# Kernel tuning notes

Hardware: AMD Instinct MI355X
Metric: run time of the kernel (lower is better)

## Reference

```python
import jax, jax.numpy as jnp
import numpy as np

B, N, DIM_IN, DIM, DIM_C, RES, PAD, NBLK = 4, 32768, 3, 128, 128, 64, 0.1, 5
R2 = RES * RES
PLANES = ((0, 2), (0, 1), (1, 2))  # xz, xy, yz as in ConvONet


def setup_inputs() -> dict:
    key = jax.random.key(0)
    ks = jax.random.split(key, 8)
    x = jax.random.uniform(ks[0], (B, N, DIM_IN), minval=-0.55, maxval=0.55, dtype=jnp.float32)
    w = lambda k, sh: (jax.random.normal(k, sh, dtype=jnp.float32) * 0.02)
    return {
        "x": x,
        "stem_w": w(ks[1], (DIM_IN, 2 * DIM)), "stem_b": jnp.zeros((2 * DIM,), jnp.float32),
        "blk_fc0_w": w(ks[2], (NBLK, 2 * DIM, DIM)), "blk_fc0_b": jnp.zeros((NBLK, DIM), jnp.float32),
        "blk_fc1_w": w(ks[3], (NBLK, DIM, DIM)), "blk_fc1_b": jnp.zeros((NBLK, DIM), jnp.float32),
        "blk_sc_w": w(ks[4], (NBLK, 2 * DIM, DIM)), "blk_sc_b": jnp.zeros((NBLK, DIM), jnp.float32),
        "fc_c_w": w(ks[5], (DIM, DIM_C)), "fc_c_b": jnp.zeros((DIM_C,), jnp.float32),
    }


def _tri_indices(xyz):
    # per-plane flat grid index, ConvONet-style normalization with padding
    idxs = []
    for (a, b) in PLANES:
        p = xyz[..., (a, b)] / (1.0 + PAD + 1e-3) + 0.5
        p = jnp.clip(p, 0.0, 1.0 - 1e-6)
        ij = jnp.clip((p * RES).astype(jnp.int32), 0, RES - 1)
        idxs.append(ij[..., 0] + RES * ij[..., 1])  # (B, N)
    return idxs


def _scatter(c, idx, reduction):
    # c: (B, N, D), idx: (B, N) -> (B, R2, D)
    b, n, d = c.shape
    seg = (idx + jnp.arange(b, dtype=idx.dtype)[:, None] * R2).reshape(-1)
    flat = c.reshape(b * n, d)
    if reduction == "max":
        out = jax.ops.segment_max(flat, seg, num_segments=b * R2)
        out = jnp.where(jnp.isfinite(out), out, jnp.zeros((), c.dtype))  # empty cells -> 0
    else:  # mean
        s = jax.ops.segment_sum(flat, seg, num_segments=b * R2)
        cnt = jax.ops.segment_sum(jnp.ones((b * n, 1), c.dtype), seg, num_segments=b * R2)
        out = s / jnp.maximum(cnt, 1.0)
    return out.reshape(b, R2, d)


def _pool_local(h, idxs):
    # scatter-max into each triplane, gather back per-point, sum over the 3 planes
    out = jnp.zeros_like(h)
    for idx in idxs:
        grid = _scatter(h, idx, "max")                       # (B, R2, D)
        out = out + jnp.take_along_axis(grid, idx[..., None], axis=1)
    return out


def _block(h, w0, b0, w1, b1, ws, bs):
    # pre-activation residual MLP (ResnetBlockFC)
    net = jax.nn.relu(h) @ w0 + b0
    dx = jax.nn.relu(net) @ w1 + b1
    return h @ ws + bs + dx


def reference(x, stem_w, stem_b, blk_fc0_w, blk_fc0_b, blk_fc1_w, blk_fc1_b,
              blk_sc_w, blk_sc_b, fc_c_w, fc_c_b):
    xyz = x[..., :3]
    idxs = _tri_indices(xyz)
    h = x @ stem_w + stem_b                                  # (B, N, 2*DIM)
    h = _block(h, blk_fc0_w[0], blk_fc0_b[0], blk_fc1_w[0], blk_fc1_b[0], blk_sc_w[0], blk_sc_b[0])
    for i in range(1, NBLK):
        h = jnp.concatenate([h, _pool_local(h, idxs)], axis=-1)
        h = _block(h, blk_fc0_w[i], blk_fc0_b[i], blk_fc1_w[i], blk_fc1_b[i], blk_sc_w[i], blk_sc_b[i])
    c = h @ fc_c_w + fc_c_b                                  # (B, N, DIM_C)
    tri = jnp.stack([_scatter(c, idx, "mean") for idx in idxs])  # (3, B, R2, DIM_C)
    # flat index = i + RES*j -> reshape gives (j, i); move channels to front
    tri = tri.reshape(3, B, RES, RES, DIM_C).transpose(0, 1, 4, 2, 3)  # (3, B, DIM_C, RES, RES)
    return (xyz, c, tri)
```

## Files before the change

kernel.cpp:

```cpp
#include <hip/hip_runtime.h>
#include <hip/hip_bf16.h>

#define B_   4
#define NPTS 32768
#define BN   131072
#define RES  64
#define R2   4096
#define DIM  128
#define K2   256
#define NBLK 5
#define NSEG (3*B_*R2)

typedef __bf16 bf16x8 __attribute__((ext_vector_type(8)));
typedef float  f32x16 __attribute__((ext_vector_type(16)));
typedef unsigned int uintv4 __attribute__((ext_vector_type(4)));

#define MFMA(a,b,c) __builtin_amdgcn_mfma_f32_32x32x16_bf16((a),(b),(c),0,0,0)

#define O_IDX  0
#define O_CNT  (O_IDX + BN*16)
#define O_OFF  (O_CNT + NSEG*4)
#define O_WOFF (O_OFF + NSEG*4)
#define O_LIST (O_WOFF + NSEG*4)
#define O_H    (O_LIST + 3*BN*4)
#define O_GRID (O_H + BN*DIM*2)
#define O_W    (O_GRID + NSEG*DIM*2)
#define WBLK_ELEMS 81920

#define OUT_C_OFF   393216
#define OUT_TRI_OFF 17170432

__device__ __forceinline__ unsigned short f2bf(float f){
  unsigned int u = __float_as_uint(f);
  return (unsigned short)((u + 0x7fffu + ((u >> 16) & 1u)) >> 16);
}
__device__ __forceinline__ float bflo(unsigned int u){ return __uint_as_float(u << 16); }
__device__ __forceinline__ float bfhi(unsigned int u){ return __uint_as_float(u & 0xffff0000u); }
__device__ __forceinline__ int coord_bin(float u){
  float p = u / 1.101f + 0.5f;
  p = fminf(fmaxf(p, 0.0f), (float)(1.0 - 1e-6));
  int i = (int)(p * 64.0f);
  return i < 0 ? 0 : (i > 63 ? 63 : i);
}
__device__ __forceinline__ unsigned int pk_relu(unsigned int a){
  unsigned int r, z = 0;
  asm("v_pk_max_f16 %0, %1, %2" : "=v"(r) : "v"(a), "v"(z));
  return r;
}
__device__ __forceinline__ bf16x8 relu8(bf16x8 v){
  uintv4 u = __builtin_bit_cast(uintv4, v);
  u[0] = pk_relu(u[0]); u[1] = pk_relu(u[1]); u[2] = pk_relu(u[2]); u[3] = pk_relu(u[3]);
  return __builtin_bit_cast(bf16x8, u);
}

__global__ void k_prep(const float* __restrict__ x, float* __restrict__ out_xyz,
                       int* __restrict__ idx4, int* __restrict__ cnt){
  int p = blockIdx.x * 256 + threadIdx.x;
  if (p >= BN) return;
  float x0 = x[p*3+0], x1 = x[p*3+1], x2 = x[p*3+2];
  out_xyz[p*3+0] = x0; out_xyz[p*3+1] = x1; out_xyz[p*3+2] = x2;
  int b = p >> 15;
  int c0 = coord_bin(x0) + 64*coord_bin(x2);
  int c1 = coord_bin(x0) + 64*coord_bin(x1);
  int c2 = coord_bin(x1) + 64*coord_bin(x2);
  int4 c4; c4.x = c0; c4.y = c1; c4.z = c2; c4.w = 0;
  *(int4*)(idx4 + p*4) = c4;
  atomicAdd(&cnt[(0*B_+b)*R2 + c0], 1);
  atomicAdd(&cnt[(1*B_+b)*R2 + c1], 1);
  atomicAdd(&cnt[(2*B_+b)*R2 + c2], 1);
}

__global__ __launch_bounds__(1024) void k_scan(const int* __restrict__ cnt,
                                               int* __restrict__ off, int* __restrict__ woff){
  __shared__ int part[1024];
  const int t = threadIdx.x;
  const int PER = NSEG / 1024;
  const int base = t * PER;
  int s = 0;
  for (int i = 0; i < PER; ++i) s += cnt[base+i];
  part[t] = s;
  __syncthreads();
  for (int d = 1; d < 1024; d <<= 1){
    int v = (t >= d) ? part[t-d] : 0;
    __syncthreads();
    part[t] += v;
    __syncthreads();
  }
  int acc = (t == 0) ? 0 : part[t-1];
  for (int i = 0; i < PER; ++i){
    int c = cnt[base+i];
    off[base+i] = acc; woff[base+i] = acc;
    acc += c;
  }
}

__global__ void k_bin(const int* __restrict__ idx4, int* __restrict__ woff, int* __restrict__ list){
  int p = blockIdx.x * 256 + threadIdx.x;
  if (p >= BN) return;
  int b = p >> 15;
  int4 c4 = *(const int4*)(idx4 + p*4);
  int cs[3] = {c4.x, c4.y, c4.z};
  #pragma unroll
  for (int pl = 0; pl < 3; ++pl){
    int s = (pl*B_+b)*R2 + cs[pl];
    int slot = atomicAdd(&woff[s], 1);
    list[slot] = p;
  }
}

__global__ void k_prepw(const float* __restrict__ fc0, const float* __restrict__ fc1,
                        const float* __restrict__ scw, const float* __restrict__ fcc,
                        unsigned short* __restrict__ wdst){
  int t = blockIdx.x * 256 + threadIdx.x;
  if (t < 163840){
    int b = t >> 15, r = t & 32767;
    int j = r & 7, l = (r >> 3) & 63, ks = (r >> 9) & 15, w = r >> 13;
    int n = w*32 + (l & 31);
    int k = ks*16 + (l >> 5)*8 + j;
    wdst[b*WBLK_ELEMS + r] = f2bf(fc0[(b*256 + k)*128 + n]);
  } else if (t < 327680){
    int t2 = t - 163840;
    int b = t2 >> 15, r = t2 & 32767;
    int j = r & 7, l = (r >> 3) & 63, ks = (r >> 9) & 15, w = r >> 13;
    int n = w*32 + (l & 31);
    int k = ks*16 + (l >> 5)*8 + j;
    wdst[b*WBLK_ELEMS + 32768 + r] = f2bf(scw[(b*256 + k)*128 + n]);
  } else if (t < 409600){
    int t2 = t - 327680;
    int b = t2 >> 14, r = t2 & 16383;
    int j = r & 7, l = (r >> 3) & 63, ks = (r >> 9) & 7, w = (r >> 12) & 3;
    int n = w*32 + (l & 31);
    int k = ks*16 + (l >> 5)*8 + j;
    wdst[b*WBLK_ELEMS + 65536 + r] = f2bf(fc1[(b*128 + k)*128 + n]);
  } else if (t < 425984){
    int r = t - 409600;
    int j = r & 7, l = (r >> 3) & 63, ks = (r >> 9) & 7, w = (r >> 12) & 3;
    int n = w*32 + (l & 31);
    int k = ks*16 + (l >> 5)*8 + j;
    wdst[5*WBLK_ELEMS + r] = f2bf(fcc[k*128 + n]);
  }
}

__global__ __launch_bounds__(256) void k_cellmax(const unsigned short* __restrict__ h,
    const int* __restrict__ off, const int* __restrict__ cnt,
    const int* __restrict__ list, unsigned short* __restrict__ gbf){
  const int seg = (blockIdx.x * 256 + threadIdx.x) >> 6;
  const int l = threadIdx.x & 63;
  const int base = off[seg], n = cnt[seg];
  float m0 = -INFINITY, m1 = -INFINITY;
  int i = 0;
  for (; i + 4 <= n; i += 4){
    int p0 = list[base+i], p1 = list[base+i+1], p2 = list[base+i+2], p3 = list[base+i+3];
    unsigned int u0 = *(const unsigned int*)(h + p0*DIM + 2*l);
    unsigned int u1 = *(const unsigned int*)(h + p1*DIM + 2*l);
    unsigned int u2 = *(const unsigned int*)(h + p2*DIM + 2*l);
    unsigned int u3 = *(const unsigned int*)(h + p3*DIM + 2*l);
    m0 = fmaxf(fmaxf(fmaxf(m0, bflo(u0)), fmaxf(bflo(u1), bflo(u2))), bflo(u3));
    m1 = fmaxf(fmaxf(fmaxf(m1, bfhi(u0)), fmaxf(bfhi(u1), bfhi(u2))), bfhi(u3));
  }
  for (; i < n; ++i){
    int p = list[base+i];
    unsigned int u = *(const unsigned int*)(h + p*DIM + 2*l);
    m0 = fmaxf(m0, bflo(u)); m1 = fmaxf(m1, bfhi(u));
  }
  unsigned int o = 0;
  if (n > 0) o = (__float_as_uint(m0) >> 16) | (__float_as_uint(m1) & 0xffff0000u);
  *(unsigned int*)(gbf + (size_t)seg*DIM + 2*l) = o;
}

template<int MODE>
__global__ __launch_bounds__(256, 4) void k_block(
    const float* __restrict__ x,
    const float* __restrict__ stem_w, const float* __restrict__ stem_b,
    unsigned short* __restrict__ h,
    const unsigned short* __restrict__ gbf, const int* __restrict__ idx4,
    const unsigned short* __restrict__ wT,
    const float* __restrict__ b0g, const float* __restrict__ b1g, const float* __restrict__ bsg)
{
  __shared__ unsigned short lh2[64*256];
  const int t = threadIdx.x;
  const int tile0 = blockIdx.x * 64;

  if (MODE == 0){
    const int dg8 = (t & 31) * 8;
    const int prow = t >> 5;
    float wa[8], wb[8], wc[8], bb[8];
    #pragma unroll
    for (int j = 0; j < 8; ++j){
      wa[j] = stem_w[dg8+j]; wb[j] = stem_w[256+dg8+j]; wc[j] = stem_w[512+dg8+j];
      bb[j] = stem_b[dg8+j];
    }
    #pragma unroll
    for (int pass = 0; pass < 8; ++pass){
      int p = prow + pass*8;
      int pg = tile0 + p;
      float x0 = x[pg*3+0], x1 = x[pg*3+1], x2 = x[pg*3+2];
      unsigned int pk[4];
      #pragma unroll
      for (int j = 0; j < 4; ++j){
        float v0 = bb[2*j]   + x0*wa[2*j]   + x1*wb[2*j]   + x2*wc[2*j];
        float v1 = bb[2*j+1] + x0*wa[2*j+1] + x1*wb[2*j+1] + x2*wc[2*j+1];
        pk[j] = (unsigned int)f2bf(v0) | ((unsigned int)f2bf(v1) << 16);
      }
      uint4 q; q.x = pk[0]; q.y = pk[1]; q.z = pk[2]; q.w = pk[3];
      *(uint4*)((char*)lh2 + p*512 + ((dg8*2) ^ ((p & 7) << 4))) = q;
    }
  } else {
    const int dg4 = (t & 31) * 4;
    const int prow = t >> 5;
    int4 cl[8];
    #pragma unroll
    for (int pass = 0; pass < 8; ++pass)
      cl[pass] = *(const int4*)(idx4 + (tile0 + prow + pass*8)*4);
    #pragma unroll
    for (int pass = 0; pass < 8; ++pass){
      int p = prow + pass*8;
      int pg = tile0 + p;
      int b = pg >> 15;
      uint2 hv = *(const uint2*)(h + pg*DIM + dg4);
      const unsigned short* g0 = gbf + ((size_t)((0*B_+b)*R2 + cl[pass].x))*DIM + dg4;
      const unsigned short* g1 = gbf + ((size_t)((1*B_+b)*R2 + cl[pass].y))*DIM + dg4;
      const unsigned short* g2 = gbf + ((size_t)((2*B_+b)*R2 + cl[pass].z))*DIM + dg4;
      uint2 v0 = *(const uint2*)g0;
      uint2 v1 = *(const uint2*)g1;
      uint2 v2 = *(const uint2*)g2;
      *(uint2*)((char*)lh2 + p*512 + ((dg4*2) ^ ((p & 7) << 4))) = hv;
      float s0 = bflo(v0.x) + bflo(v1.x) + bflo(v2.x);
      float s1 = bfhi(v0.x) + bfhi(v1.x) + bfhi(v2.x);
      float s2 = bflo(v0.y) + bflo(v1.y) + bflo(v2.y);
      float s3 = bfhi(v0.y) + bfhi(v1.y) + bfhi(v2.y);
      uint2 pv;
      pv.x = (unsigned int)f2bf(s0) | ((unsigned int)f2bf(s1) << 16);
      pv.y = (unsigned int)f2bf(s2) | ((unsigned int)f2bf(s3) << 16);
      *(uint2*)((char*)lh2 + p*512 + (((128 + dg4)*2) ^ ((p & 7) << 4))) = pv;
    }
  }
  __syncthreads();

  const int w  = t >> 6;
  const int l  = t & 63;
  const int lm = l & 31;
  const int hi = l >> 5;
  const int D0 = w * 32;
  const int swz  = (lm & 7) << 4;
  const unsigned short* w0f = wT +          ((size_t)w*16*64 + l)*8;
  const unsigned short* wsf = wT + 32768 +  ((size_t)w*16*64 + l)*8;
  const unsigned short* w1f = wT + 65536 +  ((size_t)w* 8*64 + l)*8;

  f32x16 an0, an1, as0, as1;
  #pragma unroll
  for (int i = 0; i < 16; ++i){ an0[i] = 0.f; an1[i] = 0.f; as0[i] = 0.f; as1[i] = 0.f; }

  const char* lr0 = (const char*)lh2 + lm*512;
  const char* lr1 = (const char*)lh2 + (32+lm)*512;

  #pragma unroll 4
  for (int ks = 0; ks < 16; ++ks){
    bf16x8 a0 = *(const bf16x8*)(w0f + ks*512);
    bf16x8 a1 = *(const bf16x8*)(wsf + ks*512);
    int kb = (ks*32 + hi*16) ^ swz;
    bf16x8 br0 = *(const bf16x8*)(lr0 + kb);
    bf16x8 br1 = *(const bf16x8*)(lr1 + kb);
    an0 = MFMA(a0, relu8(br0), an0);
    as0 = MFMA(a1, br0, as0);
    an1 = MFMA(a0, relu8(br1), an1);
    as1 = MFMA(a1, br1, as1);
  }

  __syncthreads();

  {
    char* nr0 = (char*)lh2 + lm*256;
    char* nr1 = (char*)lh2 + (32+lm)*256;
    #pragma unroll
    for (int g = 0; g < 4; ++g){
      int d0 = D0 + 8*g + 4*hi;
      float q0 = b0g[d0], q1 = b0g[d0+1], q2 = b0g[d0+2], q3 = b0g[d0+3];
      uint2 u0, u1;
      {
        float v0 = fmaxf(an0[4*g+0]+q0, 0.f), v1 = fmaxf(an0[4*g+1]+q1, 0.f);
        float v2 = fmaxf(an0[4*g+2]+q2, 0.f), v3 = fmaxf(an0[4*g+3]+q3, 0.f);
        u0.x = (unsigned int)f2bf(v0) | ((unsigned int)f2bf(v1) << 16);
        u0.y = (unsigned int)f2bf(v2) | ((unsigned int)f2bf(v3) << 16);
      }
      {
        float v0 = fmaxf(an1[4*g+0]+q0, 0.f), v1 = fmaxf(an1[4*g+1]+q1, 0.f);
        float v2 = fmaxf(an1[4*g+2]+q2, 0.f), v3 = fmaxf(an1[4*g+3]+q3, 0.f);
        u1.x = (unsigned int)f2bf(v0) | ((unsigned int)f2bf(v1) << 16);
        u1.y = (unsigned int)f2bf(v2) | ((unsigned int)f2bf(v3) << 16);
      }
      int ob = (d0*2) ^ swz;
      *(uint2*)(nr0 + ob) = u0;
      *(uint2*)(nr1 + ob) = u1;
    }
  }
  __syncthreads();

  f32x16 ad0, ad1;
  #pragma unroll
  for (int i = 0; i < 16; ++i){ ad0[i] = 0.f; ad1[i] = 0.f; }
  const char* nr0c = (const char*)lh2 + lm*256;
  const char* nr1c = (const char*)lh2 + (32+lm)*256;
  #pragma unroll 4
  for (int ks = 0; ks < 8; ++ks){
    bf16x8 a = *(const bf16x8*)(w1f + ks*512);
    int kb = (ks*32 + hi*16) ^ swz;
    ad0 = MFMA(a, *(const bf16x8*)(nr0c + kb), ad0);
    ad1 = MFMA(a, *(const bf16x8*)(nr1c + kb), ad1);
  }

  #pragma unroll
  for (int g = 0; g < 4; ++g){
    int d0 = D0 + 8*g + 4*hi;
    float p0 = b1g[d0]   + bsg[d0];
    float p1 = b1g[d0+1] + bsg[d0+1];
    float p2 = b1g[d0+2] + bsg[d0+2];
    float p3 = b1g[d0+3] + bsg[d0+3];
    {
      int pg = tile0 + lm;
      float v0 = as0[4*g+0]+ad0[4*g+0]+p0, v1 = as0[4*g+1]+ad0[4*g+1]+p1;
      float v2 = as0[4*g+2]+ad0[4*g+2]+p2, v3 = as0[4*g+3]+ad0[4*g+3]+p3;
      uint2 o;
      o.x = (unsigned int)f2bf(v0) | ((unsigned int)f2bf(v1) << 16);
      o.y = (unsigned int)f2bf(v2) | ((unsigned int)f2bf(v3) << 16);
      *(uint2*)(h + pg*DIM + d0) = o;
    }
    {
      int pg = tile0 + 32 + lm;
      float v0 = as1[4*g+0]+ad1[4*g+0]+p0, v1 = as1[4*g+1]+ad1[4*g+1]+p1;
      float v2 = as1[4*g+2]+ad1[4*g+2]+p2, v3 = as1[4*g+3]+ad1[4*g+3]+p3;
      uint2 o;
      o.x = (unsigned int)f2bf(v0) | ((unsigned int)f2bf(v1) << 16);
      o.y = (unsigned int)f2bf(v2) | ((unsigned int)f2bf(v3) << 16);
      *(uint2*)(h + pg*DIM + d0) = o;
    }
  }
}

__global__ __launch_bounds__(256) void k_final(
    const unsigned short* __restrict__ h,
    const unsigned short* __restrict__ fcf, const float* __restrict__ fcb,
    float* __restrict__ cout)
{
  __shared__ unsigned short lh[64*128];
  const int t = threadIdx.x;
  const int tile0 = blockIdx.x * 64;
  {
    int dg4 = (t & 31) * 4, prow = t >> 5;
    #pragma unroll
    for (int pass = 0; pass < 8; ++pass){
      int p = prow + pass*8, pg = tile0 + p;
      uint2 hv = *(const uint2*)(h + pg*DIM + dg4);
      *(uint2*)((char*)lh + p*256 + ((dg4*2) ^ ((p & 7) << 4))) = hv;
    }
  }
  __syncthreads();
  const int w = t >> 6, l = t & 63, lm = l & 31, hi = l >> 5;
  const int D0 = w*32, swz = (lm & 7) << 4;
  const unsigned short* fw = fcf + ((size_t)w*8*64 + l)*8;
  f32x16 ac0, ac1;
  #pragma unroll
  for (int i = 0; i < 16; ++i){ ac0[i] = 0.f; ac1[i] = 0.f; }
  const char* r0 = (const char*)lh + lm*256;
  const char* r1 = (const char*)lh + (32+lm)*256;
  #pragma unroll 4
  for (int ks = 0; ks < 8; ++ks){
    bf16x8 a = *(const bf16x8*)(fw + ks*512);
    int kb = (ks*32 + hi*16) ^ swz;
    ac0 = MFMA(a, *(const bf16x8*)(r0 + kb), ac0);
    ac1 = MFMA(a, *(const bf16x8*)(r1 + kb), ac1);
  }
  #pragma unroll
  for (int g = 0; g < 4; ++g){
    int d0 = D0 + 8*g + 4*hi;
    float q0 = fcb[d0], q1 = fcb[d0+1], q2 = fcb[d0+2], q3 = fcb[d0+3];
    {
      int pg = tile0 + lm;
      float4 f4;
      f4.x = ac0[4*g+0]+q0; f4.y = ac0[4*g+1]+q1; f4.z = ac0[4*g+2]+q2; f4.w = ac0[4*g+3]+q3;
      *(float4*)(cout + (size_t)pg*DIM + d0) = f4;
    }
    {
      int pg = tile0 + 32 + lm;
      float4 f4;
      f4.x = ac1[4*g+0]+q0; f4.y = ac1[4*g+1]+q1; f4.z = ac1[4*g+2]+q2; f4.w = ac1[4*g+3]+q3;
      *(float4*)(cout + (size_t)pg*DIM + d0) = f4;
    }
  }
}

__global__ __launch_bounds__(256) void k_cellsum(const float* __restrict__ c,
    const int* __restrict__ off, const int* __restrict__ cnt,
    const int* __restrict__ list, float* __restrict__ sgrid){
  const int seg = (blockIdx.x * 256 + threadIdx.x) >> 6;
  const int l = threadIdx.x & 63;
  const int base = off[seg], n = cnt[seg];
  float s0 = 0.f, s1 = 0.f;
  int i = 0;
  for (; i + 4 <= n; i += 4){
    int p0 = list[base+i], p1 = list[base+i+1], p2 = list[base+i+2], p3 = list[base+i+3];
    float2 v0 = *(const float2*)(c + (size_t)p0*DIM + 2*l);
    float2 v1 = *(const float2*)(c + (size_t)p1*DIM + 2*l);
    float2 v2 = *(const float2*)(c + (size_t)p2*DIM + 2*l);
    float2 v3 = *(const float2*)(c + (size_t)p3*DIM + 2*l);
    s0 += (v0.x + v1.x) + (v2.x + v3.x);
    s1 += (v0.y + v1.y) + (v2.y + v3.y);
  }
  for (; i < n; ++i){
    int p = list[base+i];
    float2 v = *(const float2*)(c + (size_t)p*DIM + 2*l);
    s0 += v.x; s1 += v.y;
  }
  float den = 1.0f / (float)(n < 1 ? 1 : n);
  float2 o; o.x = s0 * den; o.y = s1 * den;
  *(float2*)(sgrid + (size_t)seg*DIM + 2*l) = o;
}

__global__ __launch_bounds__(256) void k_tritr(const float* __restrict__ sgrid,
                                               float* __restrict__ tri){
  __shared__ float ls[64*129];
  const int t = threadIdx.x;
  const int wg = blockIdx.x;
  const int pl = wg >> 8;
  const int b  = (wg >> 6) & 3;
  const int r  = wg & 63;
  const int segbase = (pl*B_+b)*R2 + r*64;
  #pragma unroll 4
  for (int i = 0; i < 16; ++i){
    int f = t + i*256;
    int cell = f >> 6, d2 = f & 63;
    float2 v = *(const float2*)(sgrid + (size_t)(segbase+cell)*DIM + d2*2);
    ls[cell*129 + d2*2]   = v.x;
    ls[cell*129 + d2*2+1] = v.y;
  }
  __syncthreads();
  float* dst = tri + (size_t)((pl*B_+b)*DIM) * R2 + r*64;
  #pragma unroll 4
  for (int i = 0; i < 32; ++i){
    int li = t + i*256;
    int d = li >> 6, cc = li & 63;
    dst[(size_t)d*R2 + cc] = ls[cc*129 + d];
  }
}

extern "C" void kernel_launch(void* const* d_in, const int* in_sizes, int n_in,
                              void* d_out, int out_size, void* d_ws, size_t ws_size,
                              hipStream_t stream){
  const float* x      = (const float*)d_in[0];
  const float* stem_w = (const float*)d_in[1];
  const float* stem_b = (const float*)d_in[2];
  const float* fc0_w  = (const float*)d_in[3];
  const float* fc0_b  = (const float*)d_in[4];
  const float* fc1_w  = (const float*)d_in[5];
  const float* fc1_b  = (const float*)d_in[6];
  const float* sc_w   = (const float*)d_in[7];
  const float* sc_b   = (const float*)d_in[8];
  const float* fcc_w  = (const float*)d_in[9];
  const float* fcc_b  = (const float*)d_in[10];

  char* ws = (char*)d_ws;
  int* idx4           = (int*)(ws + O_IDX);
  int* cnt            = (int*)(ws + O_CNT);
  int* off            = (int*)(ws + O_OFF);
  int* woff           = (int*)(ws + O_WOFF);
  int* list           = (int*)(ws + O_LIST);
  unsigned short* h   = (unsigned short*)(ws + O_H);
  float* sgrid        = (float*)(ws + O_H);
  unsigned short* gbf = (unsigned short*)(ws + O_GRID);
  unsigned short* wbf = (unsigned short*)(ws + O_W);

  float* out     = (float*)d_out;
  float* out_xyz = out;
  float* out_c   = out + OUT_C_OFF;
  float* out_tri = out + OUT_TRI_OFF;

  hipMemsetAsync(cnt, 0, NSEG*4, stream);
  k_prep<<<BN/256, 256, 0, stream>>>(x, out_xyz, idx4, cnt);
  k_prepw<<<1664, 256, 0, stream>>>(fc0_w, fc1_w, sc_w, fcc_w, wbf);
  k_scan<<<1, 1024, 0, stream>>>(cnt, off, woff);
  k_bin<<<BN/256, 256, 0, stream>>>(idx4, woff, list);

  k_block<0><<<BN/64, 256, 0, stream>>>(x, stem_w, stem_b, h, nullptr, nullptr,
                                        wbf, fc0_b, fc1_b, sc_b);
  for (int i = 1; i < NBLK; ++i){
    k_cellmax<<<NSEG/4, 256, 0, stream>>>(h, off, cnt, list, gbf);
    k_block<1><<<BN/64, 256, 0, stream>>>(nullptr, nullptr, nullptr, h, gbf, idx4,
                                          wbf + (size_t)i*WBLK_ELEMS,
                                          fc0_b + i*DIM, fc1_b + i*DIM, sc_b + i*DIM);
  }
  k_final<<<BN/64, 256, 0, stream>>>(h, wbf + (size_t)5*WBLK_ELEMS, fcc_b, out_c);
  k_cellsum<<<NSEG/4, 256, 0, stream>>>(out_c, off, cnt, list, sgrid);
  k_tritr<<<768, 256, 0, stream>>>(sgrid, out_tri);
}
```

Before: 431.5 us.

## Apply final linear layer after cell-mean pooling instead of before

Because the mean is linear, the triplane features are now computed by averaging the bf16 hidden state h per cell and then applying the fc_c GEMM per cell with MFMA. Bias is masked for empty cells. This replaces the fp32 gather over out_c and the separate transpose kernel with a bf16 gather (half the bytes) plus a small per-cell GEMM that writes the transposed output directly. It adds rounding differences from bf16 averaging and rounding of the cell means before the GEMM.

```diff
diff --git a/kernel.cpp b/kernel.cpp
--- a/kernel.cpp
+++ b/kernel.cpp
@@ -389,9 +389,9 @@
   }
 }
 
-__global__ __launch_bounds__(256) void k_cellsum(const float* __restrict__ c,
+__global__ __launch_bounds__(256) void k_cellmean(const unsigned short* __restrict__ h,
     const int* __restrict__ off, const int* __restrict__ cnt,
-    const int* __restrict__ list, float* __restrict__ sgrid){
+    const int* __restrict__ list, unsigned short* __restrict__ mgrid){
   const int seg = (blockIdx.x * 256 + threadIdx.x) >> 6;
   const int l = threadIdx.x & 63;
   const int base = off[seg], n = cnt[seg];
@@ -399,47 +399,72 @@
   int i = 0;
   for (; i + 4 <= n; i += 4){
     int p0 = list[base+i], p1 = list[base+i+1], p2 = list[base+i+2], p3 = list[base+i+3];
-    float2 v0 = *(const float2*)(c + (size_t)p0*DIM + 2*l);
-    float2 v1 = *(const float2*)(c + (size_t)p1*DIM + 2*l);
-    float2 v2 = *(const float2*)(c + (size_t)p2*DIM + 2*l);
-    float2 v3 = *(const float2*)(c + (size_t)p3*DIM + 2*l);
-    s0 += (v0.x + v1.x) + (v2.x + v3.x);
-    s1 += (v0.y + v1.y) + (v2.y + v3.y);
+    unsigned int u0 = *(const unsigned int*)(h + p0*DIM + 2*l);
+    unsigned int u1 = *(const unsigned int*)(h + p1*DIM + 2*l);
+    unsigned int u2 = *(const unsigned int*)(h + p2*DIM + 2*l);
+    unsigned int u3 = *(const unsigned int*)(h + p3*DIM + 2*l);
+    s0 += (bflo(u0) + bflo(u1)) + (bflo(u2) + bflo(u3));
+    s1 += (bfhi(u0) + bfhi(u1)) + (bfhi(u2) + bfhi(u3));
   }
   for (; i < n; ++i){
     int p = list[base+i];
-    float2 v = *(const float2*)(c + (size_t)p*DIM + 2*l);
-    s0 += v.x; s1 += v.y;
+    unsigned int u = *(const unsigned int*)(h + p*DIM + 2*l);
+    s0 += bflo(u); s1 += bfhi(u);
   }
   float den = 1.0f / (float)(n < 1 ? 1 : n);
-  float2 o; o.x = s0 * den; o.y = s1 * den;
-  *(float2*)(sgrid + (size_t)seg*DIM + 2*l) = o;
-}
-
-__global__ __launch_bounds__(256) void k_tritr(const float* __restrict__ sgrid,
-                                               float* __restrict__ tri){
-  __shared__ float ls[64*129];
+  unsigned int o = (unsigned int)f2bf(s0 * den) | ((unsigned int)f2bf(s1 * den) << 16);
+  *(unsigned int*)(mgrid + (size_t)seg*DIM + 2*l) = o;
+}
+
+__global__ __launch_bounds__(256) void k_trigemm(const unsigned short* __restrict__ mgrid,
+    const unsigned short* __restrict__ fcf, const float* __restrict__ fcb,
+    const int* __restrict__ cnt, float* __restrict__ tri)
+{
+  __shared__ unsigned short lh[64*128];
   const int t = threadIdx.x;
   const int wg = blockIdx.x;
   const int pl = wg >> 8;
   const int b  = (wg >> 6) & 3;
   const int r  = wg & 63;
   const int segbase = (pl*B_+b)*R2 + r*64;
+  {
+    int dg4 = (t & 31) * 4, prow = t >> 5;
+    #pragma unroll
+    for (int pass = 0; pass < 8; ++pass){
+      int p = prow + pass*8;
+      uint2 hv = *(const uint2*)(mgrid + (size_t)(segbase + p)*DIM + dg4);
+      *(uint2*)((char*)lh + p*256 + ((dg4*2) ^ ((p & 7) << 4))) = hv;
+    }
+  }
+  __syncthreads();
+  const int w = t >> 6, l = t & 63, lm = l & 31, hi = l >> 5;
+  const int D0 = w*32, swz = (lm & 7) << 4;
+  const unsigned short* fw = fcf + ((size_t)w*8*64 + l)*8;
+  f32x16 ac0, ac1;
+  #pragma unroll
+  for (int i = 0; i < 16; ++i){ ac0[i] = 0.f; ac1[i] = 0.f; }
+  const char* r0 = (const char*)lh + lm*256;
+  const char* r1 = (const char*)lh + (32+lm)*256;
   #pragma unroll 4
-  for (int i = 0; i < 16; ++i){
-    int f = t + i*256;
-    int cell = f >> 6, d2 = f & 63;
-    float2 v = *(const float2*)(sgrid + (size_t)(segbase+cell)*DIM + d2*2);
-    ls[cell*129 + d2*2]   = v.x;
-    ls[cell*129 + d2*2+1] = v.y;
-  }
-  __syncthreads();
-  float* dst = tri + (size_t)((pl*B_+b)*DIM) * R2 + r*64;
-  #pragma unroll 4
-  for (int i = 0; i < 32; ++i){
-    int li = t + i*256;
-    int d = li >> 6, cc = li & 63;
-    dst[(size_t)d*R2 + cc] = ls[cc*129 + d];
+  for (int ks = 0; ks < 8; ++ks){
+    bf16x8 a = *(const bf16x8*)(fw + ks*512);
+    int kb = (ks*32 + hi*16) ^ swz;
+    ac0 = MFMA(a, *(const bf16x8*)(r0 + kb), ac0);
+    ac1 = MFMA(a, *(const bf16x8*)(r1 + kb), ac1);
+  }
+  float z0 = (cnt[segbase + lm]      > 0) ? 1.0f : 0.0f;
+  float z1 = (cnt[segbase + 32 + lm] > 0) ? 1.0f : 0.0f;
+  float* dst = tri + ((size_t)((pl*B_+b)*DIM)) * R2 + r*64;
+  #pragma unroll
+  for (int g = 0; g < 4; ++g){
+    int d0 = D0 + 8*g + 4*hi;
+    #pragma unroll
+    for (int j = 0; j < 4; ++j){
+      int d = d0 + j;
+      float q = fcb[d];
+      dst[(size_t)d*R2 + lm]      = (ac0[4*g+j] + q) * z0;
+      dst[(size_t)d*R2 + 32 + lm] = (ac1[4*g+j] + q) * z1;
+    }
   }
 }
 
@@ -465,7 +490,6 @@
   int* woff           = (int*)(ws + O_WOFF);
   int* list           = (int*)(ws + O_LIST);
   unsigned short* h   = (unsigned short*)(ws + O_H);
-  float* sgrid        = (float*)(ws + O_H);
   unsigned short* gbf = (unsigned short*)(ws + O_GRID);
   unsigned short* wbf = (unsigned short*)(ws + O_W);
 
@@ -489,6 +513,6 @@
                                           fc0_b + i*DIM, fc1_b + i*DIM, sc_b + i*DIM);
   }
   k_final<<<BN/64, 256, 0, stream>>>(h, wbf + (size_t)5*WBLK_ELEMS, fcc_b, out_c);
-  k_cellsum<<<NSEG/4, 256, 0, stream>>>(out_c, off, cnt, list, sgrid);
-  k_tritr<<<768, 256, 0, stream>>>(sgrid, out_tri);
-}
+  k_cellmean<<<NSEG/4, 256, 0, stream>>>(h, off, cnt, list, gbf);
+  k_trigemm<<<768, 256, 0, stream>>>(gbf, wbf + (size_t)5*WBLK_ELEMS, fcc_b, cnt, out_tri);
+}
```

Result: faster. 422.2 us (-2.2%).
